# Kernel tuning notes

Hardware: AMD Instinct MI355X
Metric: run time of the kernel (lower is better)

Reference implementation:

```python
import jax, jax.numpy as jnp
import numpy as np

UNITS, ORDER, THETA, DT = 512, 256, 784.0, 1.0


def _lmu_AB(order, theta, dt):
    # Continuous-time Legendre delay system (Voelker & Eliasmith 2018)
    Q = np.arange(order, dtype=np.float64)
    R = (2.0 * Q + 1.0)[:, None] / theta
    i, j = np.meshgrid(Q, Q, indexing='ij')
    A = np.where(i < j, -1.0, (-1.0) ** (i - j + 1)) * R
    B = ((-1.0) ** Q)[:, None] * R
    # ZOH discretization: Ad = expm(A*dt); Bd = A^{-1}(Ad - I)B
    Ad = np.asarray(jax.scipy.linalg.expm(jnp.asarray(A * dt, dtype=jnp.float64)))
    Bd = np.linalg.solve(A, (Ad - np.eye(order)) @ B)
    # cell stores AT = (Ad - I)^T so that m <- m + m@AT + u@BT
    return (Ad - np.eye(order)).T.astype(np.float32), Bd.T.astype(np.float32)


def setup_inputs() -> dict:
    key = jax.random.key(0)
    ks = jax.random.split(key, 6)
    D = 1
    x = jax.random.normal(ks[0], (64, 1024, D), dtype=jnp.float32)
    # lecun_uniform: U(-sqrt(3/fan_in), sqrt(3/fan_in))
    ie = jax.random.uniform(ks[1], (D, 1), minval=-np.sqrt(3.0 / D), maxval=np.sqrt(3.0 / D), dtype=jnp.float32)
    he = jax.random.uniform(ks[2], (UNITS, 1), minval=-np.sqrt(3.0 / UNITS), maxval=np.sqrt(3.0 / UNITS), dtype=jnp.float32)
    me = jnp.zeros((ORDER, 1), dtype=jnp.float32)  # Constant(0) initializer
    # glorot_normal: std = sqrt(2/(fan_in+fan_out))
    ik = jax.random.normal(ks[3], (D, UNITS), dtype=jnp.float32) * np.sqrt(2.0 / (D + UNITS))
    hk = jax.random.normal(ks[4], (UNITS, UNITS), dtype=jnp.float32) * np.sqrt(2.0 / (2 * UNITS))
    mk = jax.random.normal(ks[5], (ORDER, UNITS), dtype=jnp.float32) * np.sqrt(2.0 / (ORDER + UNITS))
    AT, BT = _lmu_AB(ORDER, THETA / DT, DT)
    return {"x": x, "input_encoders": ie, "hidden_encoders": he, "memory_encoders": me,
            "input_kernel": ik, "hidden_kernel": hk, "memory_kernel": mk,
            "AT": jnp.asarray(AT), "BT": jnp.asarray(BT)}


def reference(x, input_encoders, hidden_encoders, memory_encoders,
              input_kernel, hidden_kernel, memory_kernel, AT, BT):
    B = x.shape[0]
    h0 = jnp.zeros((B, UNITS), dtype=x.dtype)
    m0 = jnp.zeros((B, ORDER), dtype=x.dtype)

    def step(carry, xt):  # xt: [B, D]
        h, m = carry
        u = xt @ input_encoders + h @ hidden_encoders + m @ memory_encoders  # [B,1]
        m = m + m @ AT + u @ BT                                             # [B,order]
        h = jnp.tanh(xt @ input_kernel + h @ hidden_kernel + m @ memory_kernel)
        return (h, m), h

    xs = jnp.transpose(x, (1, 0, 2))  # [T,B,D]
    _, hs = jax.lax.scan(step, (h0, m0), xs)
    return jnp.transpose(hs, (1, 0, 2))  # [B,T,units]
```

## Files before the change

kernel.cpp:

```cpp
#include <hip/hip_runtime.h>
#include <hip/hip_fp16.h>

typedef unsigned int u32;
typedef unsigned short u16;
typedef _Float16 half2v __attribute__((ext_vector_type(2)));

#define N_UNITS 512
#define N_ORDER 256
#define N_T     1024
#define N_B     64
#define KWG     4
#define PKT_STRIDE 288

__device__ inline float dot2f(u32 a, u32 b, float acc) {
    return __builtin_amdgcn_fdot2(__builtin_bit_cast(half2v, a),
                                  __builtin_bit_cast(half2v, b), acc, false);
}
__device__ inline u16 f2h_bits(float v) {
    _Float16 f = (_Float16)v;
    return __builtin_bit_cast(u16, f);
}
__device__ inline float hbits2f(u32 dw) {
    u16 s = (u16)(dw & 0xFFFFu);
    _Float16 f = __builtin_bit_cast(_Float16, s);
    return (float)f;
}
__device__ inline u32 pack_h2(float a, float b) {
    return (u32)f2h_bits(a) | ((u32)f2h_bits(b) << 16);
}
__device__ inline u32 aload(const u32* p) {
    return __hip_atomic_load(p, __ATOMIC_RELAXED, __HIP_MEMORY_SCOPE_AGENT);
}
__device__ inline void astore(u32* p, u32 v) {
    __hip_atomic_store(p, v, __ATOMIC_RELAXED, __HIP_MEMORY_SCOPE_AGENT);
}

__global__ __launch_bounds__(256)
void prep_hk(const float* __restrict__ hk, u32* __restrict__ hk2) {
    int tid = blockIdx.x * 256 + threadIdx.x;
    int kk = tid >> 9, c = tid & 511;
    hk2[tid] = pack_h2(hk[(2 * kk) * 512 + c], hk[(2 * kk + 1) * 512 + c]);
}

__global__ __launch_bounds__(512)
void prep_amk(const float* __restrict__ mk, const float* __restrict__ at,
              const float* __restrict__ bt,
              u32* __restrict__ amk2, float* __restrict__ bmk) {
    int bj = blockIdx.x, c = threadIdx.x;
    if (bj < 128) {
        int j0 = 2 * bj, j1 = j0 + 1;
        float a0 = mk[j0 * 512 + c];
        float a1 = mk[j1 * 512 + c];
        #pragma unroll 8
        for (int k = 0; k < 256; ++k) {
            float w = mk[k * 512 + c];
            a0 = fmaf(at[j0 * 256 + k], w, a0);
            a1 = fmaf(at[j1 * 256 + k], w, a1);
        }
        amk2[bj * 512 + c] = pack_h2(a0, a1);
    } else {
        float s = 0.f;
        #pragma unroll 8
        for (int k = 0; k < 256; ++k) s = fmaf(bt[k], mk[k * 512 + c], s);
        bmk[c] = s;
    }
}

__global__ __launch_bounds__(512, 2)
void lmu_main(const float* __restrict__ x, const float* __restrict__ ie,
              const float* __restrict__ he, const float* __restrict__ me,
              const float* __restrict__ ik, const float* __restrict__ bt,
              const float* __restrict__ at,
              const u32* __restrict__ hk2, const u32* __restrict__ amk2,
              const float* __restrict__ bmk,
              u32* __restrict__ pkt, float* __restrict__ out) {
    __shared__ float xs[N_T];
    __shared__ float he_sl[128], ik_sl[128], bmk_sl[128];
    __shared__ float me_sl[64], bt_sl[64];
    __shared__ __align__(8) u16 h_h16[N_UNITS];
    __shared__ __align__(8) u16 m_hi16[N_ORDER], m_lo16[N_ORDER];
    __shared__ __align__(8) float mf[N_ORDER];
    __shared__ float zbuf[512], ampart[512];
    __shared__ float upart[4];
    __shared__ float upw[2];

    const int tid = threadIdx.x;
    const int g   = blockIdx.x;
    const int b   = g & 63;
    const int q   = g >> 6;
    const int kg  = tid >> 7;
    const int cl  = tid & 127;
    const int kg8 = tid >> 6;
    const int jl  = tid & 63;
    const int J   = 64 * q + jl;
    const int lane = tid & 63;

    for (int i = tid; i < N_T; i += 512) xs[i] = x[b * N_T + i];
    if (tid < 128) {
        he_sl[tid]  = he[128 * q + tid];
        ik_sl[tid]  = ik[128 * q + tid];
        bmk_sl[tid] = bmk[128 * q + tid];
    }
    if (tid < 64) { me_sl[tid] = me[J]; bt_sl[tid] = bt[J]; }
    h_h16[tid] = 0;
    if (tid < 256) { m_hi16[tid] = 0; m_lo16[tid] = 0; mf[tid] = 0.f; }
    if (tid < 4) upart[tid] = 0.f;
    const float ie0 = ie[0];

    u32 hk_w[64];
    #pragma unroll
    for (int i = 0; i < 64; ++i)
        hk_w[i] = hk2[(size_t)(64 * kg + i) * 512 + 128 * q + cl];
    u32 amk_w[32];
    #pragma unroll
    for (int i = 0; i < 32; ++i)
        amk_w[i] = amk2[(size_t)(32 * kg + i) * 512 + 128 * q + cl];
    float at_w[32];
    #pragma unroll
    for (int i = 0; i < 32; ++i)
        at_w[i] = at[(size_t)(32 * kg8 + i) * 256 + J];

    __syncthreads();

    const u32* h2u   = reinterpret_cast<const u32*>(h_h16);
    const u32* m_hi2 = reinterpret_cast<const u32*>(m_hi16);
    const u32* m_lo2 = reinterpret_cast<const u32*>(m_lo16);
    float* outb = out + (size_t)b * N_T * N_UNITS;

    for (int t = 0; t < N_T; ++t) {
        if (t > 0) {
            const u32 ep  = (u32)t;
            const int par = (t - 1) & 1;
            if (tid < 195) {
                int pi = (tid < 192) ? (tid >> 6) : (tid - 192);
                int q2 = pi + (pi >= q ? 1 : 0);
                const u32* base = pkt + (size_t)(par * 256 + b * 4 + q2) * PKT_STRIDE;
                if (tid < 192) {
                    int i = tid & 63;
                    u32 d0, d1, d2, d3;
                    for (;;) {
                        d0 = aload(base + 4 * i + 0);
                        d1 = aload(base + 4 * i + 1);
                        d2 = aload(base + 4 * i + 2);
                        d3 = aload(base + 4 * i + 3);
                        if (((((d0 >> 16) ^ ep) | ((d1 >> 16) ^ ep)) |
                             (((d2 >> 16) ^ ep) | ((d3 >> 16) ^ ep))) == 0) break;
                    }
                    if (i < 32) {
                        int idx = 64 * q2 + 2 * i;
                        mf[idx]         = hbits2f(d0) + hbits2f(d1);
                        m_hi16[idx]     = (u16)d0;  m_lo16[idx]     = (u16)d1;
                        mf[idx + 1]     = hbits2f(d2) + hbits2f(d3);
                        m_hi16[idx + 1] = (u16)d2;  m_lo16[idx + 1] = (u16)d3;
                    } else {
                        int idx = 128 * q2 + (4 * i - 128);
                        h_h16[idx]     = (u16)d0;
                        h_h16[idx + 1] = (u16)d1;
                        h_h16[idx + 2] = (u16)d2;
                        h_h16[idx + 3] = (u16)d3;
                    }
                } else {
                    u32 d0, d1;
                    for (;;) {
                        d0 = aload(base + 256);
                        d1 = aload(base + 257);
                        if ((((d0 >> 16) ^ ep) | ((d1 >> 16) ^ ep)) == 0) break;
                    }
                    upart[q2] = hbits2f(d0) + hbits2f(d1);
                }
            }
        }
        __syncthreads();

        {
            float z = 0.f;
            #pragma unroll
            for (int i = 0; i < 64; ++i)
                z = dot2f(h2u[64 * kg + i], hk_w[i], z);
            #pragma unroll
            for (int i = 0; i < 32; ++i) {
                u32 w = amk_w[i];
                z = dot2f(m_hi2[32 * kg + i], w, z);
                z = dot2f(m_lo2[32 * kg + i], w, z);
            }
            zbuf[tid] = z;
            float am = 0.f;
            #pragma unroll
            for (int i = 0; i < 32; ++i)
                am = fmaf(mf[32 * kg8 + i], at_w[i], am);
            ampart[tid] = am;
        }
        __syncthreads();

        float u = 0.f, mnew = 0.f, hnew = 0.f;
        u16 mhi_b = 0, mlo_b = 0;
        if (tid < 128)
            u = upart[0] + upart[1] + upart[2] + upart[3] + xs[t] * ie0;
        if (tid < 64) {
            mnew = mf[J] + u * bt_sl[tid];
            #pragma unroll
            for (int gi = 0; gi < 8; ++gi) mnew += ampart[tid + 64 * gi];
            _Float16 hi = (_Float16)mnew;
            float lo = mnew - (float)hi;
            mhi_b = __builtin_bit_cast(u16, hi);
            mlo_b = f2h_bits(lo);
            mf[J] = mnew;
            m_hi16[J] = mhi_b;
            m_lo16[J] = mlo_b;
        }
        if (tid < 128) {
            float zf = zbuf[tid] + zbuf[tid + 128] + zbuf[tid + 256] + zbuf[tid + 384]
                     + xs[t] * ik_sl[tid] + u * bmk_sl[tid];
            hnew = tanhf(zf);
            outb[(size_t)t * N_UNITS + 128 * q + tid] = hnew;
            h_h16[128 * q + tid] = f2h_bits(hnew);
        }

        if (t < N_T - 1) {
            const u32 eph = (u32)(t + 1) << 16;
            u32* myb = pkt + (size_t)((t & 1) * 256 + b * 4 + q) * PKT_STRIDE;
            if (tid < 64) {
                astore(myb + 2 * tid,     (u32)mhi_b | eph);
                astore(myb + 2 * tid + 1, (u32)mlo_b | eph);
            }
            if (tid < 128)
                astore(myb + 128 + tid, (u32)f2h_bits(hnew) | eph);

            float up = 0.f;
            if (tid < 128) {
                up = hnew * he_sl[tid];
                if (tid < 64) up = fmaf(mnew, me_sl[tid], up);
            }
            #pragma unroll
            for (int off = 32; off > 0; off >>= 1) up += __shfl_down(up, off);
            if (lane == 0 && tid < 128) upw[tid >> 6] = up;
            __syncthreads();
            if (tid == 0) {
                float myu = upw[0] + upw[1];
                upart[q] = myu;
                _Float16 hi = (_Float16)myu;
                float lo = myu - (float)hi;
                astore(myb + 256, (u32)__builtin_bit_cast(u16, hi) | eph);
                astore(myb + 257, (u32)f2h_bits(lo) | eph);
            }
        }
    }
}

extern "C" void kernel_launch(void* const* d_in, const int* in_sizes, int n_in,
                              void* d_out, int out_size, void* d_ws, size_t ws_size,
                              hipStream_t stream) {
    const float* x  = (const float*)d_in[0];
    const float* ie = (const float*)d_in[1];
    const float* he = (const float*)d_in[2];
    const float* me = (const float*)d_in[3];
    const float* ik = (const float*)d_in[4];
    const float* hk = (const float*)d_in[5];
    const float* mk = (const float*)d_in[6];
    const float* at = (const float*)d_in[7];
    const float* bt = (const float*)d_in[8];

    u32*   hk2  = (u32*)d_ws;
    u32*   amk2 = hk2 + 256 * 512;
    float* bmk  = (float*)(amk2 + 128 * 512);
    u32*   pkt  = (u32*)(bmk + 512);

    prep_hk<<<512, 256, 0, stream>>>(hk, hk2);
    prep_amk<<<129, 512, 0, stream>>>(mk, at, bt, amk2, bmk);
    lmu_main<<<N_B * KWG, 512, 0, stream>>>(x, ie, he, me, ik, bt, at,
                                            hk2, amk2, bmk, pkt, (float*)d_out);
}
```

Before: 2.887 ms.

## Overlap local partial compute with remote polling and restructure per-step sync

The thread group that depends only on the block's own h slice now computes its matvec partials while other waves poll for remote packets. Polling moves to a different wave group and reads wider chunks. The u partial is published per wave, with no extra block-wide barrier and no single-thread reduction. Shared-memory reads in the dot products are vectorised to 128-bit with four independent accumulators. This is meant to cut serialized latency on each recurrent step, at the cost of more complex packet layout and ordering assumptions.

```diff
diff --git a/kernel.cpp b/kernel.cpp
--- a/kernel.cpp
+++ b/kernel.cpp
@@ -77,23 +77,32 @@
     __shared__ float xs[N_T];
     __shared__ float he_sl[128], ik_sl[128], bmk_sl[128];
     __shared__ float me_sl[64], bt_sl[64];
-    __shared__ __align__(8) u16 h_h16[N_UNITS];
-    __shared__ __align__(8) u16 m_hi16[N_ORDER], m_lo16[N_ORDER];
-    __shared__ __align__(8) float mf[N_ORDER];
-    __shared__ float zbuf[512], ampart[512];
+    __shared__ __align__(16) u16 h_h16[N_UNITS];
+    __shared__ __align__(16) u16 m_hi16[N_ORDER], m_lo16[N_ORDER];
+    __shared__ __align__(16) float mf[N_ORDER];
+    __shared__ __align__(16) float zbuf[512], ampart[512];
     __shared__ float upart[4];
-    __shared__ float upw[2];
-
-    const int tid = threadIdx.x;
-    const int g   = blockIdx.x;
-    const int b   = g & 63;
-    const int q   = g >> 6;
-    const int kg  = tid >> 7;
-    const int cl  = tid & 127;
-    const int kg8 = tid >> 6;
-    const int jl  = tid & 63;
-    const int J   = 64 * q + jl;
+    __shared__ float upw_s[3];
+
+    const int tid  = threadIdx.x;
+    const int g    = blockIdx.x;
+    const int b    = g & 63;
+    const int q    = g >> 6;
+    const int kg   = tid >> 7;
+    const int cl   = tid & 127;
+    const int kg8  = tid >> 6;
     const int lane = tid & 63;
+    const bool is_early = (kg == q);
+
+    const int P0 = 128 * ((q + 1) & 3);
+    const int tp = tid - P0;
+    const bool is_poll = (tp >= 0 && tp < 99);
+    int ch = 0, q2 = 0;
+    if (is_poll) {
+        int pi = tp / 33;
+        ch = tp - 33 * pi;
+        q2 = pi + (pi >= q ? 1 : 0);
+    }
 
     for (int i = tid; i < N_T; i += 512) xs[i] = x[b * N_T + i];
     if (tid < 128) {
@@ -101,10 +110,11 @@
         ik_sl[tid]  = ik[128 * q + tid];
         bmk_sl[tid] = bmk[128 * q + tid];
     }
-    if (tid < 64) { me_sl[tid] = me[J]; bt_sl[tid] = bt[J]; }
+    if (tid < 64) { me_sl[tid] = me[64 * q + tid]; bt_sl[tid] = bt[64 * q + tid]; }
     h_h16[tid] = 0;
     if (tid < 256) { m_hi16[tid] = 0; m_lo16[tid] = 0; mf[tid] = 0.f; }
     if (tid < 4) upart[tid] = 0.f;
+    if (tid < 3) upw_s[tid] = 0.f;
     const float ie0 = ie[0];
 
     u32 hk_w[64];
@@ -118,88 +128,129 @@
     float at_w[32];
     #pragma unroll
     for (int i = 0; i < 32; ++i)
-        at_w[i] = at[(size_t)(32 * kg8 + i) * 256 + J];
+        at_w[i] = at[(size_t)(32 * kg8 + i) * 256 + 64 * q + lane];
 
     __syncthreads();
 
-    const u32* h2u   = reinterpret_cast<const u32*>(h_h16);
-    const u32* m_hi2 = reinterpret_cast<const u32*>(m_hi16);
-    const u32* m_lo2 = reinterpret_cast<const u32*>(m_lo16);
+    const uint4*  h4  = reinterpret_cast<const uint4*>(h_h16)  + 16 * kg;
+    const uint4*  mh4 = reinterpret_cast<const uint4*>(m_hi16) + 8 * kg;
+    const uint4*  ml4 = reinterpret_cast<const uint4*>(m_lo16) + 8 * kg;
+    const float4* mf4 = reinterpret_cast<const float4*>(mf)    + 8 * kg8;
     float* outb = out + (size_t)b * N_T * N_UNITS;
+
+    auto compute_partials = [&]() {
+        float z0 = 0.f, z1 = 0.f, z2 = 0.f, z3 = 0.f;
+        #pragma unroll
+        for (int j = 0; j < 16; ++j) {
+            uint4 h = h4[j];
+            z0 = dot2f(h.x, hk_w[4 * j + 0], z0);
+            z1 = dot2f(h.y, hk_w[4 * j + 1], z1);
+            z2 = dot2f(h.z, hk_w[4 * j + 2], z2);
+            z3 = dot2f(h.w, hk_w[4 * j + 3], z3);
+        }
+        #pragma unroll
+        for (int j = 0; j < 8; ++j) {
+            uint4 mh = mh4[j];
+            uint4 ml = ml4[j];
+            z0 = dot2f(mh.x, amk_w[4 * j + 0], z0); z0 = dot2f(ml.x, amk_w[4 * j + 0], z0);
+            z1 = dot2f(mh.y, amk_w[4 * j + 1], z1); z1 = dot2f(ml.y, amk_w[4 * j + 1], z1);
+            z2 = dot2f(mh.z, amk_w[4 * j + 2], z2); z2 = dot2f(ml.z, amk_w[4 * j + 2], z2);
+            z3 = dot2f(mh.w, amk_w[4 * j + 3], z3); z3 = dot2f(ml.w, amk_w[4 * j + 3], z3);
+        }
+        zbuf[tid] = (z0 + z1) + (z2 + z3);
+        float a0 = 0.f, a1 = 0.f, a2 = 0.f, a3 = 0.f;
+        #pragma unroll
+        for (int j = 0; j < 8; ++j) {
+            float4 m4 = mf4[j];
+            a0 = fmaf(m4.x, at_w[4 * j + 0], a0);
+            a1 = fmaf(m4.y, at_w[4 * j + 1], a1);
+            a2 = fmaf(m4.z, at_w[4 * j + 2], a2);
+            a3 = fmaf(m4.w, at_w[4 * j + 3], a3);
+        }
+        ampart[tid] = (a0 + a1) + (a2 + a3);
+    };
 
     for (int t = 0; t < N_T; ++t) {
         if (t > 0) {
-            const u32 ep  = (u32)t;
-            const int par = (t - 1) & 1;
-            if (tid < 195) {
-                int pi = (tid < 192) ? (tid >> 6) : (tid - 192);
-                int q2 = pi + (pi >= q ? 1 : 0);
-                const u32* base = pkt + (size_t)(par * 256 + b * 4 + q2) * PKT_STRIDE;
-                if (tid < 192) {
-                    int i = tid & 63;
-                    u32 d0, d1, d2, d3;
+            if (is_early) compute_partials();
+            if (is_poll) {
+                const u32 ep = (u32)t;
+                const u32* base = pkt + (size_t)(((t - 1) & 1) * 256 + b * 4 + q2) * PKT_STRIDE;
+                if (ch < 32) {
+                    const u32* p8 = base + 8 * ch;
+                    u32 d0, d1, d2, d3, d4, d5, d6, d7;
                     for (;;) {
-                        d0 = aload(base + 4 * i + 0);
-                        d1 = aload(base + 4 * i + 1);
-                        d2 = aload(base + 4 * i + 2);
-                        d3 = aload(base + 4 * i + 3);
-                        if (((((d0 >> 16) ^ ep) | ((d1 >> 16) ^ ep)) |
-                             (((d2 >> 16) ^ ep) | ((d3 >> 16) ^ ep))) == 0) break;
+                        d0 = aload(p8 + 0); d1 = aload(p8 + 1);
+                        d2 = aload(p8 + 2); d3 = aload(p8 + 3);
+                        d4 = aload(p8 + 4); d5 = aload(p8 + 5);
+                        d6 = aload(p8 + 6); d7 = aload(p8 + 7);
+                        u32 bad = ((((d0 >> 16) ^ ep) | ((d1 >> 16) ^ ep)) |
+                                   (((d2 >> 16) ^ ep) | ((d3 >> 16) ^ ep))) |
+                                  ((((d4 >> 16) ^ ep) | ((d5 >> 16) ^ ep)) |
+                                   (((d6 >> 16) ^ ep) | ((d7 >> 16) ^ ep)));
+                        if (bad == 0) break;
                     }
-                    if (i < 32) {
-                        int idx = 64 * q2 + 2 * i;
-                        mf[idx]         = hbits2f(d0) + hbits2f(d1);
-                        m_hi16[idx]     = (u16)d0;  m_lo16[idx]     = (u16)d1;
-                        mf[idx + 1]     = hbits2f(d2) + hbits2f(d3);
-                        m_hi16[idx + 1] = (u16)d2;  m_lo16[idx + 1] = (u16)d3;
+                    if (ch < 16) {
+                        int idx = 64 * q2 + 4 * ch;
+                        float4 v;
+                        v.x = hbits2f(d0) + hbits2f(d1);
+                        v.y = hbits2f(d2) + hbits2f(d3);
+                        v.z = hbits2f(d4) + hbits2f(d5);
+                        v.w = hbits2f(d6) + hbits2f(d7);
+                        *reinterpret_cast<float4*>(mf + idx) = v;
+                        u32* mhp = reinterpret_cast<u32*>(m_hi16);
+                        u32* mlp = reinterpret_cast<u32*>(m_lo16);
+                        mhp[(idx >> 1) + 0] = (d0 & 0xFFFFu) | (d2 << 16);
+                        mhp[(idx >> 1) + 1] = (d4 & 0xFFFFu) | (d6 << 16);
+                        mlp[(idx >> 1) + 0] = (d1 & 0xFFFFu) | (d3 << 16);
+                        mlp[(idx >> 1) + 1] = (d5 & 0xFFFFu) | (d7 << 16);
                     } else {
-                        int idx = 128 * q2 + (4 * i - 128);
-                        h_h16[idx]     = (u16)d0;
-                        h_h16[idx + 1] = (u16)d1;
-                        h_h16[idx + 2] = (u16)d2;
-                        h_h16[idx + 3] = (u16)d3;
+                        int i0 = (128 * q2 + 8 * ch - 128) >> 1;
+                        u32* hhp = reinterpret_cast<u32*>(h_h16);
+                        hhp[i0 + 0] = (d0 & 0xFFFFu) | (d1 << 16);
+                        hhp[i0 + 1] = (d2 & 0xFFFFu) | (d3 << 16);
+                        hhp[i0 + 2] = (d4 & 0xFFFFu) | (d5 << 16);
+                        hhp[i0 + 3] = (d6 & 0xFFFFu) | (d7 << 16);
                     }
                 } else {
-                    u32 d0, d1;
+                    const u32* p6 = base + 256;
+                    u32 d0, d1, d2, d3, d4, d5;
                     for (;;) {
-                        d0 = aload(base + 256);
-                        d1 = aload(base + 257);
-                        if ((((d0 >> 16) ^ ep) | ((d1 >> 16) ^ ep)) == 0) break;
+                        d0 = aload(p6 + 0); d1 = aload(p6 + 1); d2 = aload(p6 + 2);
+                        d3 = aload(p6 + 3); d4 = aload(p6 + 4); d5 = aload(p6 + 5);
+                        u32 bad = ((((d0 >> 16) ^ ep) | ((d1 >> 16) ^ ep)) |
+                                   (((d2 >> 16) ^ ep) | ((d3 >> 16) ^ ep))) |
+                                  (((d4 >> 16) ^ ep) | ((d5 >> 16) ^ ep));
+                        if (bad == 0) break;
                     }
-                    upart[q2] = hbits2f(d0) + hbits2f(d1);
+                    upart[q2] = (hbits2f(d0) + hbits2f(d1)) + (hbits2f(d2) + hbits2f(d3))
+                              + (hbits2f(d4) + hbits2f(d5));
                 }
             }
         }
         __syncthreads();
 
-        {
-            float z = 0.f;
+        if (!is_early || t == 0) compute_partials();
+        __syncthreads();
+
+        float u = 0.f, hnew = 0.f, mnew = 0.f;
+        u16 mhi_b = 0, mlo_b = 0;
+        if (tid < 192) {
+            u = ((upart[0] + upart[1]) + (upart[2] + upart[3]))
+              + ((upw_s[0] + upw_s[1]) + upw_s[2]) + xs[t] * ie0;
+        }
+        if (tid < 128) {
+            float zf = (zbuf[tid] + zbuf[tid + 128]) + (zbuf[tid + 256] + zbuf[tid + 384])
+                     + xs[t] * ik_sl[tid] + u * bmk_sl[tid];
+            hnew = tanhf(zf);
+            outb[(size_t)t * N_UNITS + 128 * q + tid] = hnew;
+            h_h16[128 * q + tid] = f2h_bits(hnew);
+        } else if (tid < 192) {
+            const int jl = tid - 128;
+            const int J  = 64 * q + jl;
+            mnew = mf[J] + u * bt_sl[jl];
             #pragma unroll
-            for (int i = 0; i < 64; ++i)
-                z = dot2f(h2u[64 * kg + i], hk_w[i], z);
-            #pragma unroll
-            for (int i = 0; i < 32; ++i) {
-                u32 w = amk_w[i];
-                z = dot2f(m_hi2[32 * kg + i], w, z);
-                z = dot2f(m_lo2[32 * kg + i], w, z);
-            }
-            zbuf[tid] = z;
-            float am = 0.f;
-            #pragma unroll
-            for (int i = 0; i < 32; ++i)
-                am = fmaf(mf[32 * kg8 + i], at_w[i], am);
-            ampart[tid] = am;
-        }
-        __syncthreads();
-
-        float u = 0.f, mnew = 0.f, hnew = 0.f;
-        u16 mhi_b = 0, mlo_b = 0;
-        if (tid < 128)
-            u = upart[0] + upart[1] + upart[2] + upart[3] + xs[t] * ie0;
-        if (tid < 64) {
-            mnew = mf[J] + u * bt_sl[tid];
-            #pragma unroll
-            for (int gi = 0; gi < 8; ++gi) mnew += ampart[tid + 64 * gi];
+            for (int gi = 0; gi < 8; ++gi) mnew += ampart[jl + 64 * gi];
             _Float16 hi = (_Float16)mnew;
             float lo = mnew - (float)hi;
             mhi_b = __builtin_bit_cast(u16, hi);
@@ -208,42 +259,34 @@
             m_hi16[J] = mhi_b;
             m_lo16[J] = mlo_b;
         }
-        if (tid < 128) {
-            float zf = zbuf[tid] + zbuf[tid + 128] + zbuf[tid + 256] + zbuf[tid + 384]
-                     + xs[t] * ik_sl[tid] + u * bmk_sl[tid];
-            hnew = tanhf(zf);
-            outb[(size_t)t * N_UNITS + 128 * q + tid] = hnew;
-            h_h16[128 * q + tid] = f2h_bits(hnew);
-        }
-
+
+        float up_red = 0.f;
         if (t < N_T - 1) {
             const u32 eph = (u32)(t + 1) << 16;
             u32* myb = pkt + (size_t)((t & 1) * 256 + b * 4 + q) * PKT_STRIDE;
-            if (tid < 64) {
-                astore(myb + 2 * tid,     (u32)mhi_b | eph);
-                astore(myb + 2 * tid + 1, (u32)mlo_b | eph);
+            if (tid < 128) {
+                astore(myb + 128 + tid, (u32)f2h_bits(hnew) | eph);
+            } else if (tid < 192) {
+                const int jl = tid - 128;
+                astore(myb + 2 * jl,     (u32)mhi_b | eph);
+                astore(myb + 2 * jl + 1, (u32)mlo_b | eph);
             }
-            if (tid < 128)
-                astore(myb + 128 + tid, (u32)f2h_bits(hnew) | eph);
-
             float up = 0.f;
-            if (tid < 128) {
-                up = hnew * he_sl[tid];
-                if (tid < 64) up = fmaf(mnew, me_sl[tid], up);
-            }
+            if (tid < 128)      up = hnew * he_sl[tid];
+            else if (tid < 192) up = mnew * me_sl[tid - 128];
             #pragma unroll
             for (int off = 32; off > 0; off >>= 1) up += __shfl_down(up, off);
-            if (lane == 0 && tid < 128) upw[tid >> 6] = up;
-            __syncthreads();
-            if (tid == 0) {
-                float myu = upw[0] + upw[1];
-                upart[q] = myu;
-                _Float16 hi = (_Float16)myu;
-                float lo = myu - (float)hi;
-                astore(myb + 256, (u32)__builtin_bit_cast(u16, hi) | eph);
-                astore(myb + 257, (u32)f2h_bits(lo) | eph);
+            if (lane == 0 && tid < 192) {
+                const int w = tid >> 6;
+                _Float16 hi = (_Float16)up;
+                float lo = up - (float)hi;
+                astore(myb + 256 + 2 * w,     (u32)__builtin_bit_cast(u16, hi) | eph);
+                astore(myb + 256 + 2 * w + 1, (u32)f2h_bits(lo) | eph);
+                up_red = up;
             }
         }
+        __syncthreads();
+        if (lane == 0 && tid < 192) upw_s[tid >> 6] = up_red;
     }
 }
 
```

After: 3.762 ms. 30.3% more time.

## Publish per-wave u partials directly and poll them late to drop a barrier

Applied to the files above, without the earlier changes.

Each of the two active waves now writes its own hi/lo u-partial into the packet, instead of reducing through shared memory behind a __syncthreads and letting thread 0 store. The 128 threads that need u now poll all four blocks' partials (16 words, including their own) right before u is used, rather than in the early gather phase. This removes one block-wide barrier per timestep and moves the u wait off the critical path of the dot-product phase. In exchange every consuming thread issues redundant atomic loads and spin-waits on more flag words, and the summation order of the partials changes slightly.

```diff
diff --git a/kernel.cpp b/kernel.cpp
--- a/kernel.cpp
+++ b/kernel.cpp
@@ -81,8 +81,6 @@
     __shared__ __align__(8) u16 m_hi16[N_ORDER], m_lo16[N_ORDER];
     __shared__ __align__(8) float mf[N_ORDER];
     __shared__ float zbuf[512], ampart[512];
-    __shared__ float upart[4];
-    __shared__ float upw[2];
 
     const int tid = threadIdx.x;
     const int g   = blockIdx.x;
@@ -104,7 +102,6 @@
     if (tid < 64) { me_sl[tid] = me[J]; bt_sl[tid] = bt[J]; }
     h_h16[tid] = 0;
     if (tid < 256) { m_hi16[tid] = 0; m_lo16[tid] = 0; mf[tid] = 0.f; }
-    if (tid < 4) upart[tid] = 0.f;
     const float ie0 = ie[0];
 
     u32 hk_w[64];
@@ -131,42 +128,32 @@
         if (t > 0) {
             const u32 ep  = (u32)t;
             const int par = (t - 1) & 1;
-            if (tid < 195) {
-                int pi = (tid < 192) ? (tid >> 6) : (tid - 192);
-                int q2 = pi + (pi >= q ? 1 : 0);
+            if (tid < 192) {
+                const int pi = tid >> 6;
+                const int q2 = pi + (pi >= q ? 1 : 0);
                 const u32* base = pkt + (size_t)(par * 256 + b * 4 + q2) * PKT_STRIDE;
-                if (tid < 192) {
-                    int i = tid & 63;
-                    u32 d0, d1, d2, d3;
-                    for (;;) {
-                        d0 = aload(base + 4 * i + 0);
-                        d1 = aload(base + 4 * i + 1);
-                        d2 = aload(base + 4 * i + 2);
-                        d3 = aload(base + 4 * i + 3);
-                        if (((((d0 >> 16) ^ ep) | ((d1 >> 16) ^ ep)) |
-                             (((d2 >> 16) ^ ep) | ((d3 >> 16) ^ ep))) == 0) break;
-                    }
-                    if (i < 32) {
-                        int idx = 64 * q2 + 2 * i;
-                        mf[idx]         = hbits2f(d0) + hbits2f(d1);
-                        m_hi16[idx]     = (u16)d0;  m_lo16[idx]     = (u16)d1;
-                        mf[idx + 1]     = hbits2f(d2) + hbits2f(d3);
-                        m_hi16[idx + 1] = (u16)d2;  m_lo16[idx + 1] = (u16)d3;
-                    } else {
-                        int idx = 128 * q2 + (4 * i - 128);
-                        h_h16[idx]     = (u16)d0;
-                        h_h16[idx + 1] = (u16)d1;
-                        h_h16[idx + 2] = (u16)d2;
-                        h_h16[idx + 3] = (u16)d3;
-                    }
+                const int i = tid & 63;
+                u32 d0, d1, d2, d3;
+                for (;;) {
+                    d0 = aload(base + 4 * i + 0);
+                    d1 = aload(base + 4 * i + 1);
+                    d2 = aload(base + 4 * i + 2);
+                    d3 = aload(base + 4 * i + 3);
+                    if (((((d0 >> 16) ^ ep) | ((d1 >> 16) ^ ep)) |
+                         (((d2 >> 16) ^ ep) | ((d3 >> 16) ^ ep))) == 0) break;
+                }
+                if (i < 32) {
+                    int idx = 64 * q2 + 2 * i;
+                    mf[idx]         = hbits2f(d0) + hbits2f(d1);
+                    m_hi16[idx]     = (u16)d0;  m_lo16[idx]     = (u16)d1;
+                    mf[idx + 1]     = hbits2f(d2) + hbits2f(d3);
+                    m_hi16[idx + 1] = (u16)d2;  m_lo16[idx + 1] = (u16)d3;
                 } else {
-                    u32 d0, d1;
-                    for (;;) {
-                        d0 = aload(base + 256);
-                        d1 = aload(base + 257);
-                        if ((((d0 >> 16) ^ ep) | ((d1 >> 16) ^ ep)) == 0) break;
-                    }
-                    upart[q2] = hbits2f(d0) + hbits2f(d1);
+                    int idx = 128 * q2 + (4 * i - 128);
+                    h_h16[idx]     = (u16)d0;
+                    h_h16[idx + 1] = (u16)d1;
+                    h_h16[idx + 2] = (u16)d2;
+                    h_h16[idx + 3] = (u16)d3;
                 }
             }
         }
@@ -194,8 +181,32 @@
 
         float u = 0.f, mnew = 0.f, hnew = 0.f;
         u16 mhi_b = 0, mlo_b = 0;
-        if (tid < 128)
-            u = upart[0] + upart[1] + upart[2] + upart[3] + xs[t] * ie0;
+        if (tid < 128) {
+            u = xs[t] * ie0;
+            if (t > 0) {
+                const u32 ep  = (u32)t;
+                const int par = (t - 1) & 1;
+                u32 d[16];
+                for (;;) {
+                    #pragma unroll
+                    for (int pq = 0; pq < 4; ++pq) {
+                        const u32* pp = pkt + (size_t)(par * 256 + b * 4 + pq) * PKT_STRIDE + 256;
+                        d[4 * pq + 0] = aload(pp + 0);
+                        d[4 * pq + 1] = aload(pp + 1);
+                        d[4 * pq + 2] = aload(pp + 2);
+                        d[4 * pq + 3] = aload(pp + 3);
+                    }
+                    u32 bad = 0;
+                    #pragma unroll
+                    for (int i2 = 0; i2 < 16; ++i2) bad |= (d[i2] >> 16) ^ ep;
+                    if (bad == 0) break;
+                }
+                float s = 0.f;
+                #pragma unroll
+                for (int i2 = 0; i2 < 16; ++i2) s += hbits2f(d[i2]);
+                u += s;
+            }
+        }
         if (tid < 64) {
             mnew = mf[J] + u * bt_sl[tid];
             #pragma unroll
@@ -233,15 +244,11 @@
             }
             #pragma unroll
             for (int off = 32; off > 0; off >>= 1) up += __shfl_down(up, off);
-            if (lane == 0 && tid < 128) upw[tid >> 6] = up;
-            __syncthreads();
-            if (tid == 0) {
-                float myu = upw[0] + upw[1];
-                upart[q] = myu;
-                _Float16 hi = (_Float16)myu;
-                float lo = myu - (float)hi;
-                astore(myb + 256, (u32)__builtin_bit_cast(u16, hi) | eph);
-                astore(myb + 257, (u32)f2h_bits(lo) | eph);
+            if (lane == 0 && tid < 128) {
+                _Float16 hi = (_Float16)up;
+                float lo = up - (float)hi;
+                astore(myb + 256 + 2 * (tid >> 6),     (u32)__builtin_bit_cast(u16, hi) | eph);
+                astore(myb + 256 + 2 * (tid >> 6) + 1, (u32)f2h_bits(lo) | eph);
             }
         }
     }
```

Result: slower. 3.259 ms (+12.9%).
